# Kernel optimization log

Hardware: AMD Instinct MI355X
Metric: run time of the kernel (lower is better)

The kernel has to match this reference:

```python
import jax, jax.numpy as jnp
import numpy as np

IN_F = 4096
OUT_F = 4096
RANK = 16
NUM_SLOTS = 32
ALPHA = 1.0


def setup_inputs() -> dict:
    key = jax.random.key(0)
    k_x, k_w, k_b, k_a, k_bm, k_idx = jax.random.split(key, 6)
    x = jax.random.normal(k_x, (8, 2048, IN_F), dtype=jnp.float32)
    weight = jax.random.normal(k_w, (OUT_F, IN_F), dtype=jnp.float32) * (1.0 / np.sqrt(IN_F))
    bias = jax.random.normal(k_b, (OUT_F,), dtype=jnp.float32) * 0.01
    lora_A = jax.random.normal(k_a, (NUM_SLOTS, IN_F, RANK), dtype=jnp.float32) * 1e-4
    lora_B = jax.random.normal(k_bm, (NUM_SLOTS, RANK, OUT_F), dtype=jnp.float32) * 1e-4
    lora_indices = jax.random.randint(k_idx, (8,), 0, NUM_SLOTS)
    return {"x": x, "weight": weight, "bias": bias, "lora_A": lora_A,
            "lora_B": lora_B, "lora_indices": lora_indices}


def reference(x, weight, bias, lora_A, lora_B, lora_indices):
    # base linear: x @ W.T + b
    out = jnp.einsum('bsd,od->bso', x, weight) + bias
    # per-sample LoRA slot gather + low-rank bmm chain
    chosen_A = lora_A[lora_indices]          # [B, in, r]
    chosen_B = lora_B[lora_indices]          # [B, r, out]
    inter = jnp.einsum('bsd,bdr->bsr', x, chosen_A)       # [B, S, r]
    out_lora = jnp.einsum('bsr,bro->bso', inter, chosen_B)  # [B, S, out]
    return out + ALPHA * out_lora
```

## Files before the change

### kernel.cpp

```cpp
#include <hip/hip_runtime.h>
#include <hip/hip_bf16.h>


#define M_TOT 16384
#define K_TOT 4096
#define N_TOT 4096
#define RANK 16
#define NT 128

typedef __attribute__((ext_vector_type(8))) short bf16x8;
typedef __attribute__((ext_vector_type(4))) float f32x4;

__device__ __forceinline__ unsigned short f2bf(float f) {
  unsigned int u = __builtin_bit_cast(unsigned int, f);
  u += 0x7fffu + ((u >> 16) & 1u);
  return (unsigned short)(u >> 16);
}

__global__ void cvt_bf16_kernel(const float* __restrict__ src,
                                unsigned short* __restrict__ dst, int n4) {
  int i = blockIdx.x * blockDim.x + threadIdx.x;
  const int stride = gridDim.x * blockDim.x;
  for (; i < n4; i += stride) {
    const float4 v = reinterpret_cast<const float4*>(src)[i];
    ushort4 o;
    o.x = f2bf(v.x); o.y = f2bf(v.y); o.z = f2bf(v.z); o.w = f2bf(v.w);
    reinterpret_cast<ushort4*>(dst)[i] = o;
  }
}

__global__ __launch_bounds__(256) void lora_inter_mfma_kernel(
    const unsigned short* __restrict__ xb,
    const float* __restrict__ loraA,
    const int* __restrict__ idx,
    float* __restrict__ inter) {
  const int lane = threadIdx.x & 63;
  const int wv = threadIdx.x >> 6;
  const int m0 = blockIdx.x * 64 + wv * 16;
  const int slot = idx[m0 >> 11];
  const int q = lane >> 4;
  const int c = lane & 15;
  const unsigned short* __restrict__ xrow = xb + (size_t)(m0 + c) * K_TOT + q * 8;
  const float* __restrict__ Abase = loraA + (size_t)slot * K_TOT * RANK + c;

  f32x4 acc = (f32x4){0.f, 0.f, 0.f, 0.f};
#pragma unroll 4
  for (int kt = 0; kt < K_TOT; kt += 32) {
    const bf16x8 af = *reinterpret_cast<const bf16x8*>(xrow + kt);
    const float* __restrict__ Ak = Abase + (size_t)(kt + q * 8) * RANK;
    bf16x8 bfr;
#pragma unroll
    for (int j = 0; j < 8; ++j) bfr[j] = (short)f2bf(Ak[(size_t)j * RANK]);
    acc = __builtin_amdgcn_mfma_f32_16x16x32_bf16(af, bfr, acc, 0, 0, 0);
  }
#pragma unroll
  for (int i = 0; i < 4; ++i)
    inter[(size_t)(m0 + q * 4 + i) * RANK + c] = acc[i];
}

__device__ __forceinline__ void gload16(const void* g, void* l) {
  __builtin_amdgcn_global_load_lds(
      (const __attribute__((address_space(1))) unsigned int*)g,
      (__attribute__((address_space(3))) unsigned int*)l, 16, 0, 0);
}

#define GBARRIER() asm volatile("s_barrier" ::: "memory")

__global__ __launch_bounds__(512, 2) void gemm_fused_kernel(
    const unsigned short* __restrict__ xb,
    const unsigned short* __restrict__ wb,
    const float* __restrict__ bias,
    const float* __restrict__ inter,
    const float* __restrict__ loraB,
    const int* __restrict__ idx,
    float* __restrict__ out) {
  __shared__ unsigned short lds[4][16384];
  char* ldsB = (char*)&lds[0][0];

  const int tid = threadIdx.x;
  const int lane = tid & 63;
  const int wv = tid >> 6;
  const int wr = wv >> 2;
  const int wc = wv & 3;

  const int bid = ((blockIdx.x & 7) << 7) | (blockIdx.x >> 3);
  const int m0 = (bid >> 4) << 8;
  const int n0 = (bid & 15) << 8;

  const int srow = tid >> 2;
  const int sslot = (tid & 3) ^ ((srow >> 1) & 3);
  const unsigned short* xs0 = xb + (size_t)(m0 + srow) * K_TOT + sslot * 8;
  const unsigned short* xs1 = xs0 + (size_t)128 * K_TOT;
  const unsigned short* ws0 = wb + (size_t)(n0 + srow) * K_TOT + sslot * 8;
  const unsigned short* ws1 = ws0 + (size_t)128 * K_TOT;
  const int stgoff = wv << 10;

#define STAGE_T(t)                                                  \
  do {                                                              \
    const int _bo = (((t) & 3) << 15);                              \
    gload16(xs0 + (size_t)(t) * 32, ldsB + _bo + stgoff);           \
    gload16(xs1 + (size_t)(t) * 32, ldsB + _bo + 8192 + stgoff);    \
    gload16(ws0 + (size_t)(t) * 32, ldsB + _bo + 16384 + stgoff);   \
    gload16(ws1 + (size_t)(t) * 32, ldsB + _bo + 24576 + stgoff);   \
  } while (0)

  const int rl = lane & 15;
  const int q = lane >> 4;
  const int pslot = ((q ^ ((rl >> 1) & 3)) << 4);
  const int aoff = (wr * 128 + rl) * 64 + pslot;
  const int boff = 16384 + (wc * 64 + rl) * 64 + pslot;

  f32x4 acc[8][4];
#pragma unroll
  for (int i = 0; i < 8; ++i)
#pragma unroll
    for (int j = 0; j < 4; ++j) acc[i][j] = (f32x4){0.f, 0.f, 0.f, 0.f};

  STAGE_T(0); STAGE_T(1); STAGE_T(2);
  asm volatile("s_waitcnt vmcnt(8)" ::: "memory");
  GBARRIER();

#pragma unroll 1
  for (int t = 0; t < NT; ++t) {
    const char* Ab = ldsB + ((t & 3) << 15) + aoff;
    const char* Bb = ldsB + ((t & 3) << 15) + boff;

    bf16x8 bfrag[4], afrag[8];
#pragma unroll
    for (int nf = 0; nf < 4; ++nf)
      bfrag[nf] = *reinterpret_cast<const bf16x8*>(Bb + nf * 1024);
#pragma unroll
    for (int mf = 0; mf < 8; ++mf)
      afrag[mf] = *reinterpret_cast<const bf16x8*>(Ab + mf * 1024);
    if (t < NT - 3) STAGE_T(t + 3);

    asm volatile("s_waitcnt lgkmcnt(0)" ::: "memory");
    __builtin_amdgcn_sched_barrier(0);
    __builtin_amdgcn_s_setprio(1);
#pragma unroll
    for (int mf = 0; mf < 8; ++mf)
#pragma unroll
      for (int nf = 0; nf < 4; ++nf)
        acc[mf][nf] = __builtin_amdgcn_mfma_f32_16x16x32_bf16(
            afrag[mf], bfrag[nf], acc[mf][nf], 0, 0, 0);
    __builtin_amdgcn_s_setprio(0);
    __builtin_amdgcn_sched_barrier(0);

    if (t < NT - 4) {
      asm volatile("s_waitcnt vmcnt(8)" ::: "memory");
    } else if (t == NT - 4) {
      asm volatile("s_waitcnt vmcnt(8)" ::: "memory");
    } else if (t == NT - 3) {
      asm volatile("s_waitcnt vmcnt(4)" ::: "memory");
    } else {
      asm volatile("s_waitcnt vmcnt(0)" ::: "memory");
    }
    GBARRIER();
  }

  const int slot = idx[m0 >> 11];
  const float* __restrict__ Bmat = loraB + (size_t)slot * RANK * N_TOT;
  const int gn0 = n0 + wc * 64 + rl;

  float bcv[4][RANK];
  float bv[4];
#pragma unroll
  for (int nf = 0; nf < 4; ++nf) {
    const int gn = gn0 + nf * 16;
    bv[nf] = bias[gn];
#pragma unroll
    for (int p = 0; p < RANK; ++p) bcv[nf][p] = Bmat[(size_t)p * N_TOT + gn];
  }
#pragma unroll
  for (int mf = 0; mf < 8; ++mf) {
    const int gmb = m0 + wr * 128 + mf * 16 + (q << 2);
#pragma unroll
    for (int r = 0; r < 4; ++r) {
      const int gm = gmb + r;
      const float4* ivp = reinterpret_cast<const float4*>(inter + (size_t)gm * RANK);
      const float4 iv0 = ivp[0], iv1 = ivp[1], iv2 = ivp[2], iv3 = ivp[3];
      float* orow = out + (size_t)gm * N_TOT;
#pragma unroll
      for (int nf = 0; nf < 4; ++nf) {
        const float lora =
            iv0.x * bcv[nf][0]  + iv0.y * bcv[nf][1]  + iv0.z * bcv[nf][2]  + iv0.w * bcv[nf][3] +
            iv1.x * bcv[nf][4]  + iv1.y * bcv[nf][5]  + iv1.z * bcv[nf][6]  + iv1.w * bcv[nf][7] +
            iv2.x * bcv[nf][8]  + iv2.y * bcv[nf][9]  + iv2.z * bcv[nf][10] + iv2.w * bcv[nf][11] +
            iv3.x * bcv[nf][12] + iv3.y * bcv[nf][13] + iv3.z * bcv[nf][14] + iv3.w * bcv[nf][15];
        orow[gn0 + nf * 16] = acc[mf][nf][r] + bv[nf] + lora;
      }
    }
  }
#undef STAGE_T
}

extern "C" void kernel_launch(void* const* d_in, const int* in_sizes, int n_in,
                              void* d_out, int out_size, void* d_ws, size_t ws_size,
                              hipStream_t stream) {
  const float* x     = (const float*)d_in[0];
  const float* w     = (const float*)d_in[1];
  const float* bias  = (const float*)d_in[2];
  const float* loraA = (const float*)d_in[3];
  const float* loraB = (const float*)d_in[4];
  const int*   idx   = (const int*)d_in[5];
  float* out = (float*)d_out;

  char* ws = (char*)d_ws;
  unsigned short* xb   = (unsigned short*)ws;
  unsigned short* wbuf = (unsigned short*)(ws + 134217728);
  float* inter = (float*)(ws + 134217728 + 33554432);

  cvt_bf16_kernel<<<2048, 256, 0, stream>>>(x, xb, M_TOT * K_TOT / 4);
  cvt_bf16_kernel<<<1024, 256, 0, stream>>>(w, wbuf, N_TOT * K_TOT / 4);
  lora_inter_mfma_kernel<<<M_TOT / 64, 256, 0, stream>>>(xb, loraA, idx, inter);
  gemm_fused_kernel<<<(M_TOT / 256) * (N_TOT / 256), 512, 0, stream>>>(
      xb, wbuf, bias, inter, loraB, idx, out);
}
```

Baseline: 671.8 us.

## Switch GEMM to K=64 double-buffered tiles with split LDS reads and 8-way swizzle

```diff
diff --git a/kernel.cpp b/kernel.cpp
--- a/kernel.cpp
+++ b/kernel.cpp
@@ -6,7 +6,7 @@
 #define K_TOT 4096
 #define N_TOT 4096
 #define RANK 16
-#define NT 128
+#define NT2 64
 
 typedef __attribute__((ext_vector_type(8))) short bf16x8;
 typedef __attribute__((ext_vector_type(4))) float f32x4;
@@ -65,6 +65,7 @@
 }
 
 #define GBARRIER() asm volatile("s_barrier" ::: "memory")
+#define RD(p) (*reinterpret_cast<const bf16x8*>(p))
 
 __global__ __launch_bounds__(512, 2) void gemm_fused_kernel(
     const unsigned short* __restrict__ xb,
@@ -74,7 +75,7 @@
     const float* __restrict__ loraB,
     const int* __restrict__ idx,
     float* __restrict__ out) {
-  __shared__ unsigned short lds[4][16384];
+  __shared__ unsigned short lds[2][32768];
   char* ldsB = (char*)&lds[0][0];
 
   const int tid = threadIdx.x;
@@ -87,28 +88,33 @@
   const int m0 = (bid >> 4) << 8;
   const int n0 = (bid & 15) << 8;
 
-  const int srow = tid >> 2;
-  const int sslot = (tid & 3) ^ ((srow >> 1) & 3);
-  const unsigned short* xs0 = xb + (size_t)(m0 + srow) * K_TOT + sslot * 8;
-  const unsigned short* xs1 = xs0 + (size_t)128 * K_TOT;
-  const unsigned short* ws0 = wb + (size_t)(n0 + srow) * K_TOT + sslot * 8;
-  const unsigned short* ws1 = ws0 + (size_t)128 * K_TOT;
-  const int stgoff = wv << 10;
-
-#define STAGE_T(t)                                                  \
-  do {                                                              \
-    const int _bo = (((t) & 3) << 15);                              \
-    gload16(xs0 + (size_t)(t) * 32, ldsB + _bo + stgoff);           \
-    gload16(xs1 + (size_t)(t) * 32, ldsB + _bo + 8192 + stgoff);    \
-    gload16(ws0 + (size_t)(t) * 32, ldsB + _bo + 16384 + stgoff);   \
-    gload16(ws1 + (size_t)(t) * 32, ldsB + _bo + 24576 + stgoff);   \
+  const int r0 = tid >> 3;
+  const int scol = ((tid & 7) ^ (r0 & 7)) << 3;
+  const unsigned short* xsrc = xb + (size_t)(m0 + r0) * K_TOT + scol;
+  const unsigned short* wsrc = wb + (size_t)(n0 + r0) * K_TOT + scol;
+  const int stg = tid << 4;
+
+#define STAGE64(t)                                                       \
+  do {                                                                   \
+    const int _bo = (((t) & 1) << 16);                                   \
+    const size_t _ko = (size_t)(t) * 64;                                 \
+    gload16(xsrc + _ko,                        ldsB + _bo + stg);        \
+    gload16(xsrc + (size_t)64  * K_TOT + _ko,  ldsB + _bo + 8192 + stg); \
+    gload16(xsrc + (size_t)128 * K_TOT + _ko,  ldsB + _bo + 16384 + stg);\
+    gload16(xsrc + (size_t)192 * K_TOT + _ko,  ldsB + _bo + 24576 + stg);\
+    gload16(wsrc + _ko,                        ldsB + _bo + 32768 + stg);\
+    gload16(wsrc + (size_t)64  * K_TOT + _ko,  ldsB + _bo + 40960 + stg);\
+    gload16(wsrc + (size_t)128 * K_TOT + _ko,  ldsB + _bo + 49152 + stg);\
+    gload16(wsrc + (size_t)192 * K_TOT + _ko,  ldsB + _bo + 57344 + stg);\
   } while (0)
 
   const int rl = lane & 15;
   const int q = lane >> 4;
-  const int pslot = ((q ^ ((rl >> 1) & 3)) << 4);
-  const int aoff = (wr * 128 + rl) * 64 + pslot;
-  const int boff = 16384 + (wc * 64 + rl) * 64 + pslot;
+  const int swz = rl & 7;
+  const int aoff0 = (wr * 128 + rl) * 128 + ((q ^ swz) << 4);
+  const int aoff1 = (wr * 128 + rl) * 128 + (((4 + q) ^ swz) << 4);
+  const int boff0 = 32768 + (wc * 64 + rl) * 128 + ((q ^ swz) << 4);
+  const int boff1 = 32768 + (wc * 64 + rl) * 128 + (((4 + q) ^ swz) << 4);
 
   f32x4 acc[8][4];
 #pragma unroll
@@ -116,25 +122,24 @@
 #pragma unroll
     for (int j = 0; j < 4; ++j) acc[i][j] = (f32x4){0.f, 0.f, 0.f, 0.f};
 
-  STAGE_T(0); STAGE_T(1); STAGE_T(2);
-  asm volatile("s_waitcnt vmcnt(8)" ::: "memory");
+  STAGE64(0);
+  asm volatile("s_waitcnt vmcnt(0)" ::: "memory");
   GBARRIER();
 
 #pragma unroll 1
-  for (int t = 0; t < NT; ++t) {
-    const char* Ab = ldsB + ((t & 3) << 15) + aoff;
-    const char* Bb = ldsB + ((t & 3) << 15) + boff;
-
-    bf16x8 bfrag[4], afrag[8];
-#pragma unroll
-    for (int nf = 0; nf < 4; ++nf)
-      bfrag[nf] = *reinterpret_cast<const bf16x8*>(Bb + nf * 1024);
-#pragma unroll
-    for (int mf = 0; mf < 8; ++mf)
-      afrag[mf] = *reinterpret_cast<const bf16x8*>(Ab + mf * 1024);
-    if (t < NT - 3) STAGE_T(t + 3);
-
-    asm volatile("s_waitcnt lgkmcnt(0)" ::: "memory");
+  for (int t = 0; t < NT2; ++t) {
+    const char* base = ldsB + ((t & 1) << 16);
+    bf16x8 af[8], bfr0[4], bfr1[4];
+
+#pragma unroll
+    for (int nf = 0; nf < 4; ++nf) bfr0[nf] = RD(base + boff0 + nf * 2048);
+#pragma unroll
+    for (int mf = 0; mf < 8; ++mf) af[mf] = RD(base + aoff0 + mf * 2048);
+#pragma unroll
+    for (int nf = 0; nf < 4; ++nf) bfr1[nf] = RD(base + boff1 + nf * 2048);
+    if (t < NT2 - 1) STAGE64(t + 1);
+
+    asm volatile("s_waitcnt lgkmcnt(4)" ::: "memory");
     __builtin_amdgcn_sched_barrier(0);
     __builtin_amdgcn_s_setprio(1);
 #pragma unroll
@@ -142,19 +147,25 @@
 #pragma unroll
       for (int nf = 0; nf < 4; ++nf)
         acc[mf][nf] = __builtin_amdgcn_mfma_f32_16x16x32_bf16(
-            afrag[mf], bfrag[nf], acc[mf][nf], 0, 0, 0);
+            af[mf], bfr0[nf], acc[mf][nf], 0, 0, 0);
     __builtin_amdgcn_s_setprio(0);
     __builtin_amdgcn_sched_barrier(0);
 
-    if (t < NT - 4) {
-      asm volatile("s_waitcnt vmcnt(8)" ::: "memory");
-    } else if (t == NT - 4) {
-      asm volatile("s_waitcnt vmcnt(8)" ::: "memory");
-    } else if (t == NT - 3) {
-      asm volatile("s_waitcnt vmcnt(4)" ::: "memory");
-    } else {
-      asm volatile("s_waitcnt vmcnt(0)" ::: "memory");
-    }
+#pragma unroll
+    for (int mf = 0; mf < 8; ++mf) af[mf] = RD(base + aoff1 + mf * 2048);
+    asm volatile("s_waitcnt lgkmcnt(0)" ::: "memory");
+    __builtin_amdgcn_sched_barrier(0);
+    __builtin_amdgcn_s_setprio(1);
+#pragma unroll
+    for (int mf = 0; mf < 8; ++mf)
+#pragma unroll
+      for (int nf = 0; nf < 4; ++nf)
+        acc[mf][nf] = __builtin_amdgcn_mfma_f32_16x16x32_bf16(
+            af[mf], bfr1[nf], acc[mf][nf], 0, 0, 0);
+    __builtin_amdgcn_s_setprio(0);
+    __builtin_amdgcn_sched_barrier(0);
+
+    asm volatile("s_waitcnt vmcnt(0)" ::: "memory");
     GBARRIER();
   }
 
@@ -191,7 +202,7 @@
       }
     }
   }
-#undef STAGE_T
+#undef STAGE64
 }
 
 extern "C" void kernel_launch(void* const* d_in, const int* in_sizes, int n_in,
```

Result: faster. 643.6 us (-4.2%).
